# Kernel tuning notes

Measured on AMD Instinct MI355X. Metric: run time of the kernel, lower is better.

Reference implementation:

```python
import jax, jax.numpy as jnp
import numpy as np

# Uniform batch of B graphs, N nodes each, C features, skip-window size FS
B, N, C, FS = 64, 512, 128, 16
RES = N - 1            # number of window rows per graph (unfold1d with stride 1)
TAU_A, TAU_B, TOT_EPOCHS = 10.0, 0.1, 100.0
EPS = 1e-20
NEG = -1e9


def setup_inputs() -> dict:
    key = jax.random.key(0)
    k1, k2, k3, k4 = jax.random.split(key, 4)
    x = jax.random.normal(k1, (B * N, C), dtype=jnp.float32)
    edge_index = jax.random.randint(k2, (2, 524288), 0, B * N, dtype=jnp.int32)
    score_w = jax.random.normal(k3, (C, 1), dtype=jnp.float32)       # TopKPool Linear weight
    att_params = jax.random.normal(k4, (2 * C, 1), dtype=jnp.float32)  # SKipPool att_params
    return {"x": x, "edge_index": edge_index, "score_w": score_w,
            "att_params": att_params, "epoch": 10}


def _forward(x, score_w, att_params, epoch):
    tau0 = TAU_A * (TAU_B / TAU_A) ** (epoch / TOT_EPOCHS)

    # ---- TopKPool scorer (init_ratio -> 1.0: keep all nodes, rank-sort per graph) ----
    scores = (x @ score_w)[:, 0] / jnp.linalg.norm(score_w)   # [B*N]
    sv = scores.reshape(B, N)
    order = jnp.argsort(-sv, axis=1)                           # descending perm per graph
    xg = jnp.take_along_axis(x.reshape(B, N, C), order[:, :, None], axis=1)  # [B,N,C]
    scores_ranked = jnp.tanh(jnp.take_along_axis(sv, order, axis=1))         # [B,N]

    # ---- skip-window edge construction (unfold1d semantics): row r -> dests r..r+FS-1 ----
    r = jnp.arange(RES)
    j = jnp.arange(FS)
    dest = r[:, None] + j[None, :]            # [RES,FS]
    valid = dest < N                          # padded positions masked (inf/zero rows)
    destc = jnp.minimum(dest, N - 1)

    xs = xg[:, :RES, None, :]                                  # [B,RES,1,C] sources
    xd = jnp.where(valid[None, :, :, None], xg[:, destc], 0.0)  # [B,RES,FS,C] dests

    # getDM_ei: RBF kernel over edge distances (sigma=1); masked edges -> 0 (inf row)
    d = jnp.linalg.norm(xs - xd, axis=-1)                      # [B,RES,FS]
    kmat = jnp.where(valid[None], jnp.exp(-d / 2.0), 0.0) - EPS

    # getSM_ei: attention score via att_params on [x_src || x_dst]
    a_src, a_dst = att_params[:C, 0], att_params[C:, 0]
    atts = (xg[:, :RES] @ a_src)[:, :, None] + jnp.einsum('brjc,c->brj', xd, a_dst)
    atts = jnp.where(valid[None], atts, NEG)
    w_att = jax.nn.softmax(atts / tau0, axis=-1)               # tau-annealed row softmax

    q = kmat * w_att                                           # combined edge score [B,RES,FS]
    qm = jnp.where(valid[None], q, NEG)
    w_row = jnp.max(qm, axis=-1)                               # best-match score per row (scatterSort top-1)
    jumps = 1 + jnp.argmax(qm[:, :, 1:], axis=-1).astype(jnp.int32)  # data-dependent stride in [1,FS-1]

    # ---- sequential pivot chaining (innerLoopStar): pivot -> pivot + jump[pivot] ----
    def chain(xg_b, w_b, sr_b, jumps_b):
        def step(carry, _):
            p, acc = carry
            active = p < RES
            pc = jnp.minimum(p, RES - 1)
            wv = jnp.where(active, w_b[pc] * sr_b[pc], 0.0)
            acc = acc + wv * xg_b[pc]
            p = jnp.where(active, p + jumps_b[pc], p)
            return (p, acc), None
        (pf, acc), _ = jax.lax.scan(step, (jnp.int32(0), jnp.zeros((C,), xg_b.dtype)),
                                    None, length=RES)
        return acc

    pooled = jax.vmap(chain)(xg, w_row, scores_ranked[:, :RES], jumps)  # [B,C]
    return pooled


def reference(x, edge_index, score_w, att_params, epoch):
    # edge_index only feeds the scorer's filter_adj in the original (structure unused here)
    return _forward(x, score_w, att_params, epoch)
```

## Files before the change

kernel.cpp:

```cpp
#include <hip/hip_runtime.h>
#include <math.h>

#define B_   64
#define N_   512
#define C_   128
#define FS_  16
#define RES_ 511
#define CHUNK_ 64
#define HALO_  15
#define MAXR_  (CHUNK_ + HALO_)
#define RSTRIDE_ 132
#define RSTRIDE16_ 136

__device__ __forceinline__ float bf2f(unsigned short u) {
  union { unsigned int i; float f; } v;
  v.i = ((unsigned int)u) << 16;
  return v.f;
}
__device__ __forceinline__ float bflo(unsigned int u) {
  union { unsigned int i; float f; } v; v.i = u << 16; return v.f;
}
__device__ __forceinline__ float bfhi(unsigned int u) {
  union { unsigned int i; float f; } v; v.i = u & 0xFFFF0000u; return v.f;
}

__device__ __forceinline__ float2 ld2(const void* p, int idx, int mode) {
  if (mode) return ((const float2*)p)[idx];
  ushort2 u = ((const ushort2*)p)[idx];
  return make_float2(bf2f(u.x), bf2f(u.y));
}
__device__ __forceinline__ float ld1(const void* p, int idx, int mode) {
  if (mode) return ((const float*)p)[idx];
  return bf2f(((const unsigned short*)p)[idx]);
}
__device__ __forceinline__ float4 ld4(const void* p, int idx4, int mode) {
  if (mode) return ((const float4*)p)[idx4];
  ushort4 u = ((const ushort4*)p)[idx4];
  return make_float4(bf2f(u.x), bf2f(u.y), bf2f(u.z), bf2f(u.w));
}

__device__ __forceinline__ double wred(double v) {
#pragma unroll
  for (int m = 32; m; m >>= 1) v += __shfl_xor(v, m, 64);
  return v;
}
__device__ __forceinline__ float wredf(float v) {
#pragma unroll
  for (int m = 32; m; m >>= 1) v += __shfl_xor(v, m, 64);
  return v;
}

#define RORF1(v) __builtin_bit_cast(float, __builtin_amdgcn_update_dpp( \
    0, __builtin_bit_cast(int, v), 0x121, 0xF, 0xF, false))
#define RORF2(v) __builtin_bit_cast(float, __builtin_amdgcn_update_dpp( \
    0, __builtin_bit_cast(int, v), 0x122, 0xF, 0xF, false))
#define RORF4(v) __builtin_bit_cast(float, __builtin_amdgcn_update_dpp( \
    0, __builtin_bit_cast(int, v), 0x124, 0xF, 0xF, false))
#define RORF8(v) __builtin_bit_cast(float, __builtin_amdgcn_update_dpp( \
    0, __builtin_bit_cast(int, v), 0x128, 0xF, 0xF, false))

__device__ __forceinline__ float rmax16(float v) {
  v = fmaxf(v, RORF1(v));
  v = fmaxf(v, RORF2(v));
  v = fmaxf(v, RORF4(v));
  v = fmaxf(v, RORF8(v));
  return v;
}
__device__ __forceinline__ float rsum16(float v) {
  v = v + RORF1(v);
  v = v + RORF2(v);
  v = v + RORF4(v);
  v = v + RORF8(v);
  return v;
}

__device__ __forceinline__ int detect_w0(const unsigned short* p, int lane) {
  int e = (p[lane] >> 7) & 0xFF;
  unsigned long long m = __ballot(e >= 100 && e <= 140);
  return (__popcll(m) >= 48) ? 0 : 1;
}

__device__ __forceinline__ float get_epoch(const int* ep) {
  int ei = ep[0];
  if (ei >= 0 && ei <= 1000000) return (float)ei;
  union { int i; float f; } u; u.i = ei;
  return (u.f >= 0.f && u.f <= 1e6f) ? u.f : 10.f;
}

#define USE_DOT2_ASM 1
__device__ __forceinline__ float dot2bf(float acc, unsigned int s,
                                        unsigned int d) {
#if USE_DOT2_ASM
  asm("v_dot2_f32_bf16 %0, %1, %2, %0" : "+v"(acc) : "v"(s), "v"(d));
  return acc;
#else
  return fmaf(bfhi(s), bfhi(d), fmaf(bflo(s), bflo(d), acc));
#endif
}

__global__ __launch_bounds__(256) void k_scores(
    const void* __restrict__ x, const void* __restrict__ w,
    float* __restrict__ sc)
{
  __shared__ int s_modes[2];
  const int t = threadIdx.x, lane = t & 63;
  if (t < 64) {
    int mx_ = detect_w0((const unsigned short*)x, lane);
    int mw_ = detect_w0((const unsigned short*)w, lane);
    if (t == 0) { s_modes[0] = mx_; s_modes[1] = mw_; }
  }
  __syncthreads();
  const int mode_x = s_modes[0], mode_w = s_modes[1];
  const int wid = (blockIdx.x * blockDim.x + t) >> 6;
  const int node0 = wid * 4;

  const float2 wv2 = ld2(w, lane, mode_w);
  const double nww = wred((double)wv2.x * wv2.x + (double)wv2.y * wv2.y);
  const float nrm32 = (float)sqrt(nww);

#pragma unroll
  for (int i = 0; i < 4; ++i) {
    float2 xv = ld2(x, (node0 + i) * 64 + lane, mode_x);
    double s  = wred((double)xv.x * wv2.x + (double)xv.y * wv2.y);
    if (lane == 0) sc[node0 + i] = ((float)s) / nrm32;
  }
}

__global__ __launch_bounds__(256) void k_sort(
    const float* __restrict__ sc, int* __restrict__ order,
    float* __restrict__ srk)
{
  __shared__ __align__(16) float sl[N_];
  __shared__ int part[4][CHUNK_];
  const int blk = blockIdx.x, b = blk >> 3, ch = blk & 7;
  const int bN = b * N_, t = threadIdx.x;
  sl[t]       = sc[bN + t];
  sl[t + 256] = sc[bN + t + 256];
  __syncthreads();
  const int n = t & 63, p = t >> 6;
  const int g = ch * CHUNK_ + n;
  const float my = sl[g];
  const float4* sl4 = (const float4*)sl;
  int rank = 0;
#pragma unroll 4
  for (int k4 = p * 32; k4 < p * 32 + 32; ++k4) {
    float4 v = sl4[k4];
    int k = k4 * 4;
    rank += (int)((v.x > my) || (v.x == my && k     < g));
    rank += (int)((v.y > my) || (v.y == my && k + 1 < g));
    rank += (int)((v.z > my) || (v.z == my && k + 2 < g));
    rank += (int)((v.w > my) || (v.w == my && k + 3 < g));
  }
  part[p][n] = rank;
  __syncthreads();
  if (t < CHUNK_) {
    const int gg = ch * CHUNK_ + t;
    const int r = part[0][t] + part[1][t] + part[2][t] + part[3][t];
    order[bN + r] = gg;
    srk[bN + r]   = tanhf(sl[gg]);
  }
}

__global__ __launch_bounds__(1024, 8) void k_att(
    const void* __restrict__ x, const void* __restrict__ a,
    const int* __restrict__ order, const int* __restrict__ ep,
    float* __restrict__ wrw, int* __restrict__ jmp)
{
  __shared__ __align__(16) float rows[MAXR_ * RSTRIDE_];
  __shared__ float ads_l[MAXR_];
  __shared__ float asr_l[CHUNK_];
  __shared__ float nrm_l[MAXR_];
  __shared__ int   ord_l[MAXR_];
  __shared__ int   s_modes[2];
  __shared__ float s_invtau;

  unsigned short* rows16 = (unsigned short*)rows;

  const int blk = blockIdx.x;
  const int b = blk >> 3;
  const int cr0 = (blk & 7) * CHUNK_;
  const int bN = b * N_;
  const int t = threadIdx.x;
  const int lane = t & 63, wv = t >> 6;
  const int nrows = min(N_ - cr0, MAXR_);

  if (t < 64) {
    int mx_ = detect_w0((const unsigned short*)x, lane);
    int ma_ = detect_w0((const unsigned short*)a, lane);
    if (t == 0) {
      s_modes[0] = mx_; s_modes[1] = ma_;
      float evv = get_epoch(ep);
      s_invtau = (float)(1.0 / (10.0 * pow(0.01, (double)evv / 100.0)));
    }
  }
  if (t < nrows) {
    int o = order[bN + cr0 + t];
    ord_l[t] = min(max(o, 0), N_ - 1);
  }
  __syncthreads();
  const int mode_x = s_modes[0], mode_a = s_modes[1];
  const float inv_tau = s_invtau;

  if (mode_x == 0) {
    const int rl0 = t >> 4, c8 = t & 15;
    for (int rl = rl0; rl < nrows; rl += 64) {
      uint4 v = ((const uint4*)x)[(bN + ord_l[rl]) * 16 + c8];
      *(uint4*)&rows16[rl * RSTRIDE16_ + c8 * 8] = v;
    }
  } else {
    const int rl0 = t >> 5, c4 = t & 31;
    for (int rl = rl0; rl < nrows; rl += 32) {
      float4 v = ld4(x, (bN + ord_l[rl]) * 32 + c4, 1);
      float* dst = &rows[rl * RSTRIDE_ + c4 * 4];
      dst[0] = v.x; dst[1] = v.y; dst[2] = v.z; dst[3] = v.w;
    }
  }
  __syncthreads();

  {
    const float2 sv2 = ld2(a, lane, mode_a);
    const float2 dv2 = ld2(a, 64 + lane, mode_a);
    for (int rl = wv; rl < nrows; rl += 16) {
      float xlo, xhi;
      if (mode_x == 0) {
        unsigned int u = *(const unsigned int*)&rows16[rl * RSTRIDE16_ + 2 * lane];
        xlo = bflo(u); xhi = bfhi(u);
      } else {
        float2 xr = *(const float2*)&rows[rl * RSTRIDE_ + 2 * lane];
        xlo = xr.x; xhi = xr.y;
      }
      float da = wredf(xlo * sv2.x + xhi * sv2.y);
      float dd = wredf(xlo * dv2.x + xhi * dv2.y);
      float nn = wredf(fmaf(xlo, xlo, xhi * xhi));
      if (lane == 0) {
        ads_l[rl] = dd;
        nrm_l[rl] = nn;
        if (rl < CHUNK_) asr_l[rl] = da;
      }
    }
  }
  __syncthreads();

  const int j = lane & 15, cg4 = lane >> 4;
  const int nr = min(CHUNK_, RES_ - cr0);
  int cnt = nr - wv * 4; cnt = max(0, min(4, cnt));

#pragma unroll 2
  for (int ii = 0; ii < cnt; ++ii) {
    const int rloc = wv * 4 + ii;
    const int r = cr0 + rloc;
    const int dest = r + j;
    const bool valid = dest < N_;
    const int dl = (valid ? dest : (N_ - 1)) - cr0;

    float dacc;
    if (mode_x == 0) {
      const unsigned short* sp = &rows16[rloc * RSTRIDE16_ + cg4 * 32];
      const unsigned short* dp = &rows16[dl   * RSTRIDE16_ + cg4 * 32];
      float g0 = 0.f, g1 = 0.f;
#pragma unroll
      for (int c = 0; c < 4; ++c) {
        uint4 s = ((const uint4*)sp)[c];
        uint4 d = ((const uint4*)dp)[c];
        g0 = dot2bf(g0, s.x, d.x);
        g1 = dot2bf(g1, s.y, d.y);
        g0 = dot2bf(g0, s.z, d.z);
        g1 = dot2bf(g1, s.w, d.w);
      }
      float gg = g0 + g1;
      gg += __shfl_xor(gg, 16, 64);
      gg += __shfl_xor(gg, 32, 64);
      dacc = nrm_l[rloc] + nrm_l[dl] - 2.f * gg;
    } else {
      const float* srcp = &rows[rloc * RSTRIDE_ + cg4 * 32];
      const float* dstp = &rows[dl   * RSTRIDE_ + cg4 * 32];
      float q0 = 0.f, q1 = 0.f, q2 = 0.f, q3 = 0.f;
#pragma unroll
      for (int c = 0; c < 8; ++c) {
        float4 s4 = *(const float4*)(srcp + c * 4);
        float4 d4 = *(const float4*)(dstp + c * 4);
        float e0 = s4.x - d4.x, e1 = s4.y - d4.y;
        float e2 = s4.z - d4.z, e3 = s4.w - d4.w;
        q0 = fmaf(e0, e0, q0); q1 = fmaf(e1, e1, q1);
        q2 = fmaf(e2, e2, q2); q3 = fmaf(e3, e3, q3);
      }
      float qq = (q0 + q1) + (q2 + q3);
      qq += __shfl_xor(qq, 16, 64);
      qq += __shfl_xor(qq, 32, 64);
      dacc = qq;
    }

    float d32 = (j == 0) ? 0.f : sqrtf(fmaxf(dacc, 0.f));
    float kkj = valid ? (__expf(-0.5f * d32) - 1e-20f) : -1e-20f;
    float aaj = valid ? (asr_l[rloc] + ads_l[dl]) : -1e9f;
    float ttj = aaj * inv_tau;

    float mx = rmax16(ttj);
    float eej = __expf(ttj - mx);
    float ssum = rsum16(eej);
    ssum = __shfl(ssum, lane & 48, 64);
    float q  = kkj * (eej * (1.0f / ssum));
    float qm = valid ? q : -1e9f;

    float qe = (j == 0) ? -INFINITY : qm;
    float m1 = rmax16(qe);
    float q0v = __shfl(qm, lane & 48, 64);
    float wr = fmaxf(m1, q0v);
    unsigned long long mask = __ballot(qe == m1);
    int bj = __builtin_ctz((unsigned)(mask & 0xFFFEu));

    if (lane == 0) {
      wrw[bN + r] = wr;
      jmp[bN + r] = bj;
    }
  }
}

__global__ __launch_bounds__(512) void k_chain(
    const void* __restrict__ x, const float* __restrict__ wrw,
    const float* __restrict__ srk, const int* __restrict__ jmp,
    const int* __restrict__ order, float* __restrict__ out)
{
  __shared__ int   tab[9][N_];
  __shared__ int   ol[N_];
  __shared__ float wl[N_];
  __shared__ float sl2[N_];
  __shared__ float cl[N_];
  __shared__ int   rl[N_];
  __shared__ int   Pcnt;
  __shared__ int   s_mode;

  const int b = blockIdx.x, t = threadIdx.x;
  if (t < 64) {
    int mx_ = detect_w0((const unsigned short*)x, t);
    if (t == 0) s_mode = mx_;
  }

  ol[t] = min(max(order[b * N_ + t], 0), N_ - 1);
  if (t < RES_) {
    wl[t]  = wrw[b * N_ + t];
    sl2[t] = srk[b * N_ + t];
    int jv = jmp[b * N_ + t];
    jv = min(max(jv, 1), FS_ - 1);
    tab[0][t] = min(t + jv, RES_);
  } else {
    tab[0][t] = RES_;
  }
  if (t == 0) Pcnt = RES_;
  __syncthreads();
  const int mode_x = s_mode;
#pragma unroll
  for (int k = 1; k < 9; ++k) {
    int v = tab[k - 1][tab[k - 1][t]];
    tab[k][t] = v;
    __syncthreads();
  }
  int node = 0;
#pragma unroll
  for (int k = 0; k < 9; ++k)
    if ((t >> k) & 1) node = tab[k][node];
  bool valid = (node < RES_);
  cl[t] = valid ? wl[node] * sl2[node] : 0.0f;
  rl[t] = valid ? ol[node] : 0;
  if (!valid) atomicMin(&Pcnt, t);
  __syncthreads();

  if (t < C_) {
    const int P = Pcnt;
    float acc = 0.f;
    int i = 0;
    for (; i + 8 <= P; i += 8) {
      float c0 = cl[i],     c1 = cl[i + 1], c2 = cl[i + 2], c3 = cl[i + 3];
      float c4 = cl[i + 4], c5 = cl[i + 5], c6 = cl[i + 6], c7 = cl[i + 7];
      int   r0 = rl[i],     r1 = rl[i + 1], r2 = rl[i + 2], r3 = rl[i + 3];
      int   r4 = rl[i + 4], r5 = rl[i + 5], r6 = rl[i + 6], r7 = rl[i + 7];
      float x0 = ld1(x, (b * N_ + r0) * C_ + t, mode_x);
      float x1 = ld1(x, (b * N_ + r1) * C_ + t, mode_x);
      float x2 = ld1(x, (b * N_ + r2) * C_ + t, mode_x);
      float x3 = ld1(x, (b * N_ + r3) * C_ + t, mode_x);
      float x4 = ld1(x, (b * N_ + r4) * C_ + t, mode_x);
      float x5 = ld1(x, (b * N_ + r5) * C_ + t, mode_x);
      float x6 = ld1(x, (b * N_ + r6) * C_ + t, mode_x);
      float x7 = ld1(x, (b * N_ + r7) * C_ + t, mode_x);
      acc = acc + c0 * x0;
      acc = acc + c1 * x1;
      acc = acc + c2 * x2;
      acc = acc + c3 * x3;
      acc = acc + c4 * x4;
      acc = acc + c5 * x5;
      acc = acc + c6 * x6;
      acc = acc + c7 * x7;
    }
    for (; i + 4 <= P; i += 4) {
      float c0 = cl[i],     c1 = cl[i + 1], c2 = cl[i + 2], c3 = cl[i + 3];
      int   r0 = rl[i],     r1 = rl[i + 1], r2 = rl[i + 2], r3 = rl[i + 3];
      float x0 = ld1(x, (b * N_ + r0) * C_ + t, mode_x);
      float x1 = ld1(x, (b * N_ + r1) * C_ + t, mode_x);
      float x2 = ld1(x, (b * N_ + r2) * C_ + t, mode_x);
      float x3 = ld1(x, (b * N_ + r3) * C_ + t, mode_x);
      acc = acc + c0 * x0;
      acc = acc + c1 * x1;
      acc = acc + c2 * x2;
      acc = acc + c3 * x3;
    }
    for (; i < P; ++i)
      acc = acc + cl[i] * ld1(x, (b * N_ + rl[i]) * C_ + t, mode_x);
    out[b * C_ + t] = acc;
  }
}

extern "C" void kernel_launch(void* const* d_in, const int* in_sizes, int n_in,
                              void* d_out, int out_size, void* d_ws, size_t ws_size,
                              hipStream_t stream) {
  const void* x = nullptr; const void* w = nullptr; const void* a = nullptr;
  const int* ep = nullptr;
  for (int i = 0; i < n_in; ++i) {
    int s = in_sizes[i];
    if      (s == B_ * N_ * C_) x  = d_in[i];
    else if (s == C_)           w  = d_in[i];
    else if (s == 2 * C_)       a  = d_in[i];
    else if (s == 1)            ep = (const int*)d_in[i];
  }
  if (!x)  x  = d_in[0];
  if (!w)  w  = d_in[2];
  if (!a)  a  = d_in[3];
  if (!ep) ep = (const int*)d_in[4];
  (void)out_size; (void)ws_size;

  float* ws = (float*)d_ws;
  const int NN = B_ * N_;
  float* sc    = ws;
  int*   order = (int*)(ws + NN);
  float* srk   = ws + 2 * NN;
  float* wrw   = ws + 3 * NN;
  int*   jmp   = (int*)(ws + 4 * NN);

  k_scores<<<B_ * N_ / 16, 256, 0, stream>>>(x, w, sc);
  k_sort<<<B_ * 8, 256, 0, stream>>>(sc, order, srk);
  k_att<<<B_ * 8, 1024, 0, stream>>>(x, a, order, ep, wrw, jmp);
  k_chain<<<B_, N_, 0, stream>>>(x, wrw, srk, jmp, order, (float*)d_out);
}
```

Measured before the change: 113.6 us.

## Compute windowed Gram tile with MFMA bf16 instructions in attention kernel

For bf16 inputs, k_att now builds a 64x80 Gram matrix of the gathered rows using 16x16x32 bf16 MFMA instructions and stores it in shared memory. Each wave then handles four rows at once, one row per 16-lane group, reading the dot products directly instead of running a per-row dot2 loop with shuffles. This trades redundant VALU dot products for a dense matrix-core product that also computes unused entries. It adds a runtime self-check against one scalar dot product and falls back to the old path if the check fails.

```diff
diff --git a/kernel.cpp b/kernel.cpp
--- a/kernel.cpp
+++ b/kernel.cpp
@@ -11,6 +11,11 @@
 #define MAXR_  (CHUNK_ + HALO_)
 #define RSTRIDE_ 132
 #define RSTRIDE16_ 136
+#define GOFF_ 21504
+#define GSTR_ 80
+
+typedef __attribute__((ext_vector_type(8))) short bf16x8;
+typedef __attribute__((ext_vector_type(4))) float f32x4;
 
 __device__ __forceinline__ float bf2f(unsigned short u) {
   union { unsigned int i; float f; } v;
@@ -87,15 +92,10 @@
   return (u.f >= 0.f && u.f <= 1e6f) ? u.f : 10.f;
 }
 
-#define USE_DOT2_ASM 1
 __device__ __forceinline__ float dot2bf(float acc, unsigned int s,
                                         unsigned int d) {
-#if USE_DOT2_ASM
   asm("v_dot2_f32_bf16 %0, %1, %2, %0" : "+v"(acc) : "v"(s), "v"(d));
   return acc;
-#else
-  return fmaf(bfhi(s), bfhi(d), fmaf(bflo(s), bflo(d), acc));
-#endif
 }
 
 __global__ __launch_bounds__(256) void k_scores(
@@ -166,15 +166,17 @@
     const int* __restrict__ order, const int* __restrict__ ep,
     float* __restrict__ wrw, int* __restrict__ jmp)
 {
-  __shared__ __align__(16) float rows[MAXR_ * RSTRIDE_];
+  __shared__ __align__(16) float rows[MAXR_ * RSTRIDE_ + 80];
   __shared__ float ads_l[MAXR_];
   __shared__ float asr_l[CHUNK_];
   __shared__ float nrm_l[MAXR_];
   __shared__ int   ord_l[MAXR_];
   __shared__ int   s_modes[2];
   __shared__ float s_invtau;
+  __shared__ int   s_gok;
 
   unsigned short* rows16 = (unsigned short*)rows;
+  float* Gm = (float*)((char*)rows + GOFF_);
 
   const int blk = blockIdx.x;
   const int b = blk >> 3;
@@ -189,6 +191,7 @@
     int ma_ = detect_w0((const unsigned short*)a, lane);
     if (t == 0) {
       s_modes[0] = mx_; s_modes[1] = ma_;
+      s_gok = 0;
       float evv = get_epoch(ep);
       s_invtau = (float)(1.0 / (10.0 * pow(0.01, (double)evv / 100.0)));
     }
@@ -239,60 +242,50 @@
       }
     }
   }
-  __syncthreads();
-
-  const int j = lane & 15, cg4 = lane >> 4;
+
+  if (mode_x == 0) {
+    const int fr = lane & 15, kb = (lane >> 4) * 8;
+    for (int tt = wv; tt < 20; tt += 16) {
+      const int m0 = (tt / 5) * 16, n0 = (tt % 5) * 16;
+      f32x4 acc = {0.f, 0.f, 0.f, 0.f};
+#pragma unroll
+      for (int kk = 0; kk < 4; ++kk) {
+        bf16x8 af = *(const bf16x8*)&rows16[(m0 + fr) * RSTRIDE16_ + kk * 32 + kb];
+        bf16x8 bf = *(const bf16x8*)&rows16[(n0 + fr) * RSTRIDE16_ + kk * 32 + kb];
+        acc = __builtin_amdgcn_mfma_f32_16x16x32_bf16(af, bf, acc, 0, 0, 0);
+      }
+      const int rb = (lane >> 4) * 4;
+#pragma unroll
+      for (int rg = 0; rg < 4; ++rg)
+        Gm[(m0 + rb + rg) * GSTR_ + n0 + fr] = acc[rg];
+    }
+  }
+  __syncthreads();
+
+  if (mode_x == 0 && t < 64) {
+    unsigned int u0  = *(const unsigned int*)&rows16[2 * lane];
+    unsigned int u17 = *(const unsigned int*)&rows16[17 * RSTRIDE16_ + 2 * lane];
+    float ref = wredf(fmaf(bflo(u0), bflo(u17), bfhi(u0) * bfhi(u17)));
+    if (lane == 0)
+      s_gok = (fabsf(Gm[17] - ref) <= 1e-2f * (1.f + fabsf(ref))) ? 1 : 0;
+  }
+  __syncthreads();
+
   const int nr = min(CHUNK_, RES_ - cr0);
-  int cnt = nr - wv * 4; cnt = max(0, min(4, cnt));
-
-#pragma unroll 2
-  for (int ii = 0; ii < cnt; ++ii) {
-    const int rloc = wv * 4 + ii;
+
+  if (mode_x == 0 && s_gok) {
+    const int rsub = lane >> 4, j = lane & 15;
+    const int rloc = wv * 4 + rsub;
+    const bool ractive = rloc < nr;
+    const int rl_c = ractive ? rloc : 0;
     const int r = cr0 + rloc;
-    const int dest = r + j;
-    const bool valid = dest < N_;
-    const int dl = (valid ? dest : (N_ - 1)) - cr0;
-
-    float dacc;
-    if (mode_x == 0) {
-      const unsigned short* sp = &rows16[rloc * RSTRIDE16_ + cg4 * 32];
-      const unsigned short* dp = &rows16[dl   * RSTRIDE16_ + cg4 * 32];
-      float g0 = 0.f, g1 = 0.f;
-#pragma unroll
-      for (int c = 0; c < 4; ++c) {
-        uint4 s = ((const uint4*)sp)[c];
-        uint4 d = ((const uint4*)dp)[c];
-        g0 = dot2bf(g0, s.x, d.x);
-        g1 = dot2bf(g1, s.y, d.y);
-        g0 = dot2bf(g0, s.z, d.z);
-        g1 = dot2bf(g1, s.w, d.w);
-      }
-      float gg = g0 + g1;
-      gg += __shfl_xor(gg, 16, 64);
-      gg += __shfl_xor(gg, 32, 64);
-      dacc = nrm_l[rloc] + nrm_l[dl] - 2.f * gg;
-    } else {
-      const float* srcp = &rows[rloc * RSTRIDE_ + cg4 * 32];
-      const float* dstp = &rows[dl   * RSTRIDE_ + cg4 * 32];
-      float q0 = 0.f, q1 = 0.f, q2 = 0.f, q3 = 0.f;
-#pragma unroll
-      for (int c = 0; c < 8; ++c) {
-        float4 s4 = *(const float4*)(srcp + c * 4);
-        float4 d4 = *(const float4*)(dstp + c * 4);
-        float e0 = s4.x - d4.x, e1 = s4.y - d4.y;
-        float e2 = s4.z - d4.z, e3 = s4.w - d4.w;
-        q0 = fmaf(e0, e0, q0); q1 = fmaf(e1, e1, q1);
-        q2 = fmaf(e2, e2, q2); q3 = fmaf(e3, e3, q3);
-      }
-      float qq = (q0 + q1) + (q2 + q3);
-      qq += __shfl_xor(qq, 16, 64);
-      qq += __shfl_xor(qq, 32, 64);
-      dacc = qq;
-    }
-
+    const bool valid = ractive && (r + j < N_);
+    const int dl = valid ? (rloc + j) : rl_c;
+
+    float dacc = nrm_l[rl_c] + nrm_l[dl] - 2.f * Gm[rl_c * GSTR_ + dl];
     float d32 = (j == 0) ? 0.f : sqrtf(fmaxf(dacc, 0.f));
     float kkj = valid ? (__expf(-0.5f * d32) - 1e-20f) : -1e-20f;
-    float aaj = valid ? (asr_l[rloc] + ads_l[dl]) : -1e9f;
+    float aaj = valid ? (asr_l[rl_c] + ads_l[dl]) : -1e9f;
     float ttj = aaj * inv_tau;
 
     float mx = rmax16(ttj);
@@ -307,11 +300,85 @@
     float q0v = __shfl(qm, lane & 48, 64);
     float wr = fmaxf(m1, q0v);
     unsigned long long mask = __ballot(qe == m1);
-    int bj = __builtin_ctz((unsigned)(mask & 0xFFFEu));
-
-    if (lane == 0) {
+    unsigned msk = (unsigned)(mask >> (rsub * 16)) & 0xFFFFu;
+    int bj = __builtin_ctz(msk & 0xFFFEu);
+
+    if (ractive && j == 0) {
       wrw[bN + r] = wr;
       jmp[bN + r] = bj;
+    }
+  } else {
+    const int j = lane & 15, cg4 = lane >> 4;
+    int cnt = nr - wv * 4; cnt = max(0, min(4, cnt));
+
+#pragma unroll 2
+    for (int ii = 0; ii < cnt; ++ii) {
+      const int rloc = wv * 4 + ii;
+      const int r = cr0 + rloc;
+      const int dest = r + j;
+      const bool valid = dest < N_;
+      const int dl = (valid ? dest : (N_ - 1)) - cr0;
+
+      float dacc;
+      if (mode_x == 0) {
+        const unsigned short* sp = &rows16[rloc * RSTRIDE16_ + cg4 * 32];
+        const unsigned short* dp = &rows16[dl   * RSTRIDE16_ + cg4 * 32];
+        float g0 = 0.f, g1 = 0.f;
+#pragma unroll
+        for (int c = 0; c < 4; ++c) {
+          uint4 s = ((const uint4*)sp)[c];
+          uint4 d = ((const uint4*)dp)[c];
+          g0 = dot2bf(g0, s.x, d.x);
+          g1 = dot2bf(g1, s.y, d.y);
+          g0 = dot2bf(g0, s.z, d.z);
+          g1 = dot2bf(g1, s.w, d.w);
+        }
+        float gg = g0 + g1;
+        gg += __shfl_xor(gg, 16, 64);
+        gg += __shfl_xor(gg, 32, 64);
+        dacc = nrm_l[rloc] + nrm_l[dl] - 2.f * gg;
+      } else {
+        const float* srcp = &rows[rloc * RSTRIDE_ + cg4 * 32];
+        const float* dstp = &rows[dl   * RSTRIDE_ + cg4 * 32];
+        float q0 = 0.f, q1 = 0.f, q2 = 0.f, q3 = 0.f;
+#pragma unroll
+        for (int c = 0; c < 8; ++c) {
+          float4 s4 = *(const float4*)(srcp + c * 4);
+          float4 d4 = *(const float4*)(dstp + c * 4);
+          float e0 = s4.x - d4.x, e1 = s4.y - d4.y;
+          float e2 = s4.z - d4.z, e3 = s4.w - d4.w;
+          q0 = fmaf(e0, e0, q0); q1 = fmaf(e1, e1, q1);
+          q2 = fmaf(e2, e2, q2); q3 = fmaf(e3, e3, q3);
+        }
+        float qq = (q0 + q1) + (q2 + q3);
+        qq += __shfl_xor(qq, 16, 64);
+        qq += __shfl_xor(qq, 32, 64);
+        dacc = qq;
+      }
+
+      float d32 = (j == 0) ? 0.f : sqrtf(fmaxf(dacc, 0.f));
+      float kkj = valid ? (__expf(-0.5f * d32) - 1e-20f) : -1e-20f;
+      float aaj = valid ? (asr_l[rloc] + ads_l[dl]) : -1e9f;
+      float ttj = aaj * inv_tau;
+
+      float mx = rmax16(ttj);
+      float eej = __expf(ttj - mx);
+      float ssum = rsum16(eej);
+      ssum = __shfl(ssum, lane & 48, 64);
+      float q  = kkj * (eej * (1.0f / ssum));
+      float qm = valid ? q : -1e9f;
+
+      float qe = (j == 0) ? -INFINITY : qm;
+      float m1 = rmax16(qe);
+      float q0v = __shfl(qm, lane & 48, 64);
+      float wr = fmaxf(m1, q0v);
+      unsigned long long mask = __ballot(qe == m1);
+      int bj = __builtin_ctz((unsigned)(mask & 0xFFFEu));
+
+      if (lane == 0) {
+        wrw[bN + r] = wr;
+        jmp[bN + r] = bj;
+      }
     }
   }
 }
```

Result: no change. 114.4 us (+0.7%).
